# Performance work log

Measured on AMD Instinct MI355X. Metric: run time of the kernel, lower is better.

Reference implementation:

```python
import jax, jax.numpy as jnp
import numpy as np

N, E, G = 4096, 65536, 64
C_IN, PE_DIM, H, L, HEADS, C_OUT = 64, 24, 128, 2, 4, 10
HD = H // HEADS


def setup_inputs() -> dict:
    key = jax.random.key(0)
    ks = iter(jax.random.split(key, 64))

    def nrm(shape, scale=0.05):
        return jax.random.normal(next(ks), shape, jnp.float32) * scale

    inp = {}
    inp["x"] = jax.random.normal(next(ks), (N, C_IN), jnp.float32)
    inp["lap_pe"] = jax.random.normal(next(ks), (N, 8), jnp.float32)
    inp["rw_pe"] = jax.random.normal(next(ks), (N, 16), jnp.float32)
    inp["edge_index"] = jax.random.randint(next(ks), (2, E), 0, N)
    inp["batch"] = jnp.sort(jax.random.randint(next(ks), (N,), 0, G))
    inp["Wp"] = nrm((C_IN + PE_DIM, H)); inp["bp"] = jnp.zeros((H,), jnp.float32)
    inp["gin_W1"] = nrm((L, H, H)); inp["gin_b1"] = jnp.zeros((L, H), jnp.float32)
    inp["gin_W2"] = nrm((L, H, H)); inp["gin_b2"] = jnp.zeros((L, H), jnp.float32)
    inp["bn1_g"] = jnp.ones((L, H), jnp.float32); inp["bn1_b"] = jnp.zeros((L, H), jnp.float32)
    inp["bn2_g"] = jnp.ones((L, H), jnp.float32); inp["bn2_b"] = jnp.zeros((L, H), jnp.float32)
    inp["bn3_g"] = jnp.ones((L, H), jnp.float32); inp["bn3_b"] = jnp.zeros((L, H), jnp.float32)
    inp["attn_in_w"] = nrm((L, H, 3 * H)); inp["attn_in_b"] = jnp.zeros((L, 3 * H), jnp.float32)
    inp["attn_out_w"] = nrm((L, H, H)); inp["attn_out_b"] = jnp.zeros((L, H), jnp.float32)
    inp["mlp_W1"] = nrm((L, H, 2 * H)); inp["mlp_b1"] = jnp.zeros((L, 2 * H), jnp.float32)
    inp["mlp_W2"] = nrm((L, 2 * H, H)); inp["mlp_b2"] = jnp.zeros((L, H), jnp.float32)
    inp["Wr1"] = nrm((H, H)); inp["br1"] = jnp.zeros((H,), jnp.float32)
    inp["Wr2"] = nrm((H, H)); inp["br2"] = jnp.zeros((H,), jnp.float32)
    inp["Wc"] = nrm((H, C_OUT)); inp["bc"] = jnp.zeros((C_OUT,), jnp.float32)
    return inp


def _bn(x, g, b):
    # BatchNorm1d over node dim, training-mode batch statistics (biased var)
    m = jnp.mean(x, axis=0)
    v = jnp.var(x, axis=0)
    return (x - m) * jax.lax.rsqrt(v + 1e-5) * g + b


def reference(x, lap_pe, rw_pe, edge_index, batch, Wp, bp,
              gin_W1, gin_b1, gin_W2, gin_b2,
              bn1_g, bn1_b, bn2_g, bn2_b, bn3_g, bn3_b,
              attn_in_w, attn_in_b, attn_out_w, attn_out_b,
              mlp_W1, mlp_b1, mlp_W2, mlp_b2,
              Wr1, br1, Wr2, br2, Wc, bc):
    pe = jnp.concatenate([lap_pe, rw_pe], axis=-1)          # [N, 24]
    h = jnp.concatenate([x, pe], axis=-1) @ Wp + bp         # [N, H]
    src, dst = edge_index[0], edge_index[1]
    scale = 1.0 / np.sqrt(HD)
    for l in range(L):
        # --- local GINConv: (1+eps)*x_i + sum_{j->i} x_j, eps=0, then 2-layer MLP ---
        agg = jax.ops.segment_sum(h[src], dst, num_segments=N)
        g = h + agg
        g = jax.nn.relu(g @ gin_W1[l] + gin_b1[l]) @ gin_W2[l] + gin_b2[l]
        g = _bn(g + h, bn1_g[l], bn1_b[l])                  # residual + norm1
        # --- global MHA; batch is NOT forwarded to GPSConv, so all N nodes form one dense graph ---
        qkv = h @ attn_in_w[l] + attn_in_b[l]               # [N, 3H]
        q, k, v = jnp.split(qkv, 3, axis=-1)
        q = q.reshape(N, HEADS, HD).transpose(1, 0, 2)      # [Hh, N, d]
        k = k.reshape(N, HEADS, HD).transpose(1, 0, 2)
        v = v.reshape(N, HEADS, HD).transpose(1, 0, 2)
        a = jax.nn.softmax(jnp.einsum('hnd,hmd->hnm', q, k) * scale, axis=-1)
        o = jnp.einsum('hnm,hmd->hnd', a, v).transpose(1, 0, 2).reshape(N, H)
        o = o @ attn_out_w[l] + attn_out_b[l]
        o = _bn(o + h, bn2_g[l], bn2_b[l])                  # residual + norm2
        # --- combine + FFN (channels -> 2*channels -> channels) + norm3 ---
        out = g + o
        m = jax.nn.relu(out @ mlp_W1[l] + mlp_b1[l]) @ mlp_W2[l] + mlp_b2[l]
        out = _bn(out + m, bn3_g[l], bn3_b[l])
        h = jax.nn.relu(out)                                # outer F.relu in GraphGPS
    pooled = jax.ops.segment_sum(h, batch, num_segments=G)  # global_add_pool
    r = jax.nn.relu(pooled @ Wr1 + br1)
    r = jax.nn.relu(r @ Wr2 + br2)                          # dropout(0.5) disabled (eval)
    return r @ Wc + bc                                      # [G, C_OUT]
```

## Files before the change

kernel.cpp:

```cpp
#include <hip/hip_runtime.h>
#include <hip/hip_bf16.h>
#include <math.h>

#define NN 4096
#define HH 128
#define EE 65536
#define GG 64
#define KSPLIT 8
#define KLEN (NN / KSPLIT)
#define SMEM_GEMM 14336

typedef unsigned short u16;
typedef unsigned int u32;
typedef __bf16 bf16x8 __attribute__((ext_vector_type(8)));
typedef float f32x4 __attribute__((ext_vector_type(4)));

__device__ inline u16 f2b(float f) {
  u32 u = __float_as_uint(f);
  u += 0x7FFFu + ((u >> 16) & 1u);
  return (u16)(u >> 16);
}
__device__ inline u32 pkbf2(float a, float b) {
  __hip_bfloat162 h = __float22bfloat162_rn(float2{a, b});
  u32 u; __builtin_memcpy(&u, &h, 4); return u;
}

struct TDesc { const float* src; int Ks, K, M, off; };
struct TPack { TDesc d[13]; };

__global__ __launch_bounds__(256) void transcount_k(TPack P, u16* __restrict__ dst,
    const int* __restrict__ ei, int* cnt) {
  if (blockIdx.x >= 1344) {
    int e = (blockIdx.x - 1344)*256 + threadIdx.x;
    atomicAdd(&cnt[ei[EE + e]], 1);
    return;
  }
  int idx = blockIdx.x * 256 + threadIdx.x;
  for (int i = 0; i < 13; i++) {
    int sz = P.d[i].K * P.d[i].M;
    if (idx < sz) {
      int m = idx / P.d[i].K;
      int k = idx - m * P.d[i].K;
      float v = (k < P.d[i].Ks) ? P.d[i].src[(size_t)k * P.d[i].M + m] : 0.f;
      dst[P.d[i].off + idx] = f2b(v);
      return;
    }
    idx -= sz;
  }
}

__global__ __launch_bounds__(256) void scan_k(const int* __restrict__ cnt,
    int* __restrict__ rowptr, int* __restrict__ cursor) {
  __shared__ int tot[256];
  int t = threadIdx.x;
  int base = t * 16;
  int loc[16]; int s = 0;
  #pragma unroll
  for (int i = 0; i < 16; i++) { loc[i] = s; s += cnt[base + i]; }
  tot[t] = s;
  __syncthreads();
  for (int off = 1; off < 256; off <<= 1) {
    int v = (t >= off) ? tot[t - off] : 0;
    __syncthreads();
    tot[t] += v;
    __syncthreads();
  }
  int excl = (t == 0) ? 0 : tot[t - 1];
  #pragma unroll
  for (int i = 0; i < 16; i++) {
    int p = excl + loc[i];
    rowptr[base + i] = p; cursor[base + i] = p;
  }
  if (t == 255) rowptr[NN] = excl + s;
}

__global__ __launch_bounds__(256) void aggcsr_k(const int* __restrict__ rowptr,
    const int* __restrict__ elist, const float* __restrict__ h,
    float* __restrict__ agg) {
  int d = blockIdx.x*2 + (threadIdx.x >> 7);
  int c = threadIdx.x & 127;
  int beg = rowptr[d], end = rowptr[d + 1];
  float acc = 0.f;
  for (int j = beg; j < end; j++)
    acc += h[(size_t)elist[j]*HH + c];
  agg[(size_t)d*HH + c] = acc;
}

struct GArgs {
  const float *A, *A2, *A3;
  const u16* Bt;
  const float* bias;
  float* C;
  const float *res, *res2;
  float* stats;
  const float *sbase, *pg1, *pb1, *pg2, *pb2;
  const u16 *opart;
  const float *lpart;
  u16 *qb, *kb, *vt;
  int K, M;
};

template <int ASTAGE, int EPI, int RELU>
__device__ void mgemm_dev(const GArgs& a, int bx, int by, char* smem) {
  char* Ab = smem;
  char* Bb = smem + 4096;
  float* affs = (float*)(smem + 12288);
  const int tid = threadIdx.x;
  const int n0 = bx * 32, m0 = by * 64;
  const int w = tid >> 6, lane = tid & 63;
  const int g = lane >> 4, li = lane & 15;
  const int wr = w >> 1, wc = w & 1;
  const int K = a.K, M = a.M;

  if (ASTAGE == 2) {
    int plane = tid >> 7, cc = tid & 127;
    const float* st = a.sbase + plane*256;
    const float* gg = plane ? a.pg2 : a.pg1;
    const float* bb = plane ? a.pb2 : a.pb1;
    float mean = st[cc] * (1.f/NN);
    float var  = st[128+cc] * (1.f/NN) - mean*mean;
    float s = rsqrtf(var + 1e-5f) * gg[cc];
    affs[plane*256 + cc]       = s;
    affs[plane*256 + 128 + cc] = bb[cc] - mean*s;
    __syncthreads();
  }

  f32x4 acc0 = {0,0,0,0}, acc1 = {0,0,0,0};
  const int arow = tid >> 3, akseg = (tid & 7) * 8;
  const int bcol = tid >> 2, bkseg = (tid & 3) * 16;

  for (int k0 = 0; k0 < K; k0 += 64) {
    {
      float4 a0 = {0,0,0,0}, a1 = {0,0,0,0};
      if (ASTAGE == 4) {
        int n = n0 + arow;
        if (k0 == 0) {
          a0 = *(const float4*)&a.A[(size_t)n*64 + akseg];
          a1 = *(const float4*)&a.A[(size_t)n*64 + akseg + 4];
        } else {
          if (akseg == 0)       { a0 = *(const float4*)&a.A2[(size_t)n*8];
                                  a1 = *(const float4*)&a.A2[(size_t)n*8 + 4]; }
          else if (akseg == 8)  { a0 = *(const float4*)&a.A3[(size_t)n*16];
                                  a1 = *(const float4*)&a.A3[(size_t)n*16 + 4]; }
          else if (akseg == 16) { a0 = *(const float4*)&a.A3[(size_t)n*16 + 8];
                                  a1 = *(const float4*)&a.A3[(size_t)n*16 + 12]; }
        }
      } else if (ASTAGE == 3) {
        int n = n0 + arow, c = k0 + akseg;
        int head = c >> 5, d0 = c & 31;
        float4 o0 = {0,0,0,0}, o1 = {0,0,0,0}; float L = 0.f;
        #pragma unroll
        for (int s = 0; s < KSPLIT; s++) {
          const u16* ob = a.opart + ((size_t)(s*4+head)*NN + n)*32 + d0;
          uint4 xx = *(const uint4*)ob;
          o0.x += __uint_as_float(xx.x << 16);
          o0.y += __uint_as_float(xx.x & 0xffff0000u);
          o0.z += __uint_as_float(xx.y << 16);
          o0.w += __uint_as_float(xx.y & 0xffff0000u);
          o1.x += __uint_as_float(xx.z << 16);
          o1.y += __uint_as_float(xx.z & 0xffff0000u);
          o1.z += __uint_as_float(xx.w << 16);
          o1.w += __uint_as_float(xx.w & 0xffff0000u);
          L += a.lpart[(size_t)(s*4+head)*NN + n];
        }
        float inv = 1.f / L;
        a0 = make_float4(o0.x*inv, o0.y*inv, o0.z*inv, o0.w*inv);
        a1 = make_float4(o1.x*inv, o1.y*inv, o1.z*inv, o1.w*inv);
      } else {
        const float* ap = a.A + (size_t)(n0 + arow) * K + k0 + akseg;
        a0 = *(const float4*)ap; a1 = *(const float4*)(ap + 4);
        if (ASTAGE == 1) {
          const float* p2 = a.A2 + (size_t)(n0 + arow) * K + k0 + akseg;
          float4 c0 = *(const float4*)p2, c1 = *(const float4*)(p2 + 4);
          a0.x += c0.x; a0.y += c0.y; a0.z += c0.z; a0.w += c0.w;
          a1.x += c1.x; a1.y += c1.y; a1.z += c1.z; a1.w += c1.w;
        } else if (ASTAGE == 2) {
          const float* p2 = a.A2 + (size_t)(n0 + arow) * K + k0 + akseg;
          float4 c0 = *(const float4*)p2, c1 = *(const float4*)(p2 + 4);
          const float* af = affs + k0 + akseg;
          float4 s1a = *(const float4*)af,         s1b = *(const float4*)(af + 4);
          float4 t1a = *(const float4*)(af + 128), t1b = *(const float4*)(af + 132);
          float4 s2a = *(const float4*)(af + 256), s2b = *(const float4*)(af + 260);
          float4 t2a = *(const float4*)(af + 384), t2b = *(const float4*)(af + 388);
          a0.x = a0.x*s1a.x + t1a.x + c0.x*s2a.x + t2a.x;
          a0.y = a0.y*s1a.y + t1a.y + c0.y*s2a.y + t2a.y;
          a0.z = a0.z*s1a.z + t1a.z + c0.z*s2a.z + t2a.z;
          a0.w = a0.w*s1a.w + t1a.w + c0.w*s2a.w + t2a.w;
          a1.x = a1.x*s1b.x + t1b.x + c1.x*s2b.x + t2b.x;
          a1.y = a1.y*s1b.y + t1b.y + c1.y*s2b.y + t2b.y;
          a1.z = a1.z*s1b.z + t1b.z + c1.z*s2b.z + t2b.z;
          a1.w = a1.w*s1b.w + t1b.w + c1.w*s2b.w + t2b.w;
        }
      }
      u16 t8[8] = {f2b(a0.x), f2b(a0.y), f2b(a0.z), f2b(a0.w),
                   f2b(a1.x), f2b(a1.y), f2b(a1.z), f2b(a1.w)};
      *(uint4*)(Ab + ((arow*128 + akseg*2) ^ ((arow & 7) << 4))) = *(uint4*)t8;
    }
    {
      const u16* bp = a.Bt + (size_t)(m0 + bcol) * K + k0 + bkseg;
      uint4 b0 = *(const uint4*)bp;
      uint4 b1 = *(const uint4*)(bp + 8);
      int ba = bcol*128 + bkseg*2;
      int sw = (bcol & 7) << 4;
      *(uint4*)(Bb + (ba ^ sw)) = b0;
      *(uint4*)(Bb + ((ba + 16) ^ sw)) = b1;
    }
    __syncthreads();
    int row = wr*16 + li;
    int cAl = wc*32 + li, cBl = cAl + 16;
    #pragma unroll
    for (int ck = 0; ck < 2; ck++) {
      bf16x8 af = *(const bf16x8*)(Ab + ((row*128 + ck*64 + g*16) ^ ((row & 7) << 4)));
      bf16x8 bf0 = *(const bf16x8*)(Bb + ((cAl*128 + ck*64 + g*16) ^ ((cAl & 7) << 4)));
      bf16x8 bf1 = *(const bf16x8*)(Bb + ((cBl*128 + ck*64 + g*16) ^ ((cBl & 7) << 4)));
      acc0 = __builtin_amdgcn_mfma_f32_16x16x32_bf16(af, bf0, acc0, 0, 0, 0);
      acc1 = __builtin_amdgcn_mfma_f32_16x16x32_bf16(af, bf1, acc1, 0, 0, 0);
    }
    __syncthreads();
  }

  const int colA = m0 + wc*32 + li, colB = colA + 16;
  const int colAl = wc*32 + li, colBl = colAl + 16;
  const int rbase = n0 + wr*16 + 4*g;

  if (EPI == 0) {
    float b0 = a.bias[colA], b1 = a.bias[colB];
    #pragma unroll
    for (int r = 0; r < 4; r++) {
      float v0 = acc0[r] + b0, v1 = acc1[r] + b1;
      if (RELU) { v0 = fmaxf(v0, 0.f); v1 = fmaxf(v1, 0.f); }
      a.C[(size_t)(rbase + r) * M + colA] = v0;
      a.C[(size_t)(rbase + r) * M + colB] = v1;
    }
  } else if (EPI == 1 || EPI == 3) {
    float b0 = a.bias[colA], b1 = a.bias[colB];
    float sA1=0, tA1=0, sA2=0, tA2=0, sB1=0, tB1=0, sB2=0, tB2=0;
    if (EPI == 3) {
      auto mk = [&](int col, float& s1, float& t1, float& s2, float& t2) {
        float m1 = a.sbase[col]*(1.f/NN), v1 = a.sbase[128+col]*(1.f/NN) - m1*m1;
        s1 = rsqrtf(v1 + 1e-5f) * a.pg1[col]; t1 = a.pb1[col] - m1*s1;
        float m2 = a.sbase[256+col]*(1.f/NN), v2 = a.sbase[384+col]*(1.f/NN) - m2*m2;
        s2 = rsqrtf(v2 + 1e-5f) * a.pg2[col]; t2 = a.pb2[col] - m2*s2;
      };
      mk(colA, sA1, tA1, sA2, tA2);
      mk(colB, sB1, tB1, sB2, tB2);
    }
    float s0 = 0, q0 = 0, s1 = 0, q1 = 0;
    #pragma unroll
    for (int r = 0; r < 4; r++) {
      int rw2 = rbase + r;
      float v0, v1;
      if (EPI == 1) {
        v0 = acc0[r] + b0 + a.res[(size_t)rw2 * 128 + colA];
        v1 = acc1[r] + b1 + a.res[(size_t)rw2 * 128 + colB];
      } else {
        v0 = acc0[r] + b0 + a.res[(size_t)rw2*128 + colA]*sA1 + tA1
                          + a.res2[(size_t)rw2*128 + colA]*sA2 + tA2;
        v1 = acc1[r] + b1 + a.res[(size_t)rw2*128 + colB]*sB1 + tB1
                          + a.res2[(size_t)rw2*128 + colB]*sB2 + tB2;
      }
      a.C[(size_t)rw2 * M + colA] = v0;
      a.C[(size_t)rw2 * M + colB] = v1;
      s0 += v0; q0 += v0*v0; s1 += v1; q1 += v1*v1;
    }
    s0 += __shfl_xor(s0, 16); s0 += __shfl_xor(s0, 32);
    q0 += __shfl_xor(q0, 16); q0 += __shfl_xor(q0, 32);
    s1 += __shfl_xor(s1, 16); s1 += __shfl_xor(s1, 32);
    q1 += __shfl_xor(q1, 16); q1 += __shfl_xor(q1, 32);
    float* sred = (float*)smem;
    if (lane < 16) {
      sred[wr*64 + colAl] = s0;  sred[128 + wr*64 + colAl] = q0;
      sred[wr*64 + colBl] = s1;  sred[128 + wr*64 + colBl] = q1;
    }
    __syncthreads();
    if (tid < 128) {
      int c = tid & 63, isq = tid >> 6;
      float v = sred[isq*128 + c] + sred[isq*128 + 64 + c];
      atomicAdd(&a.stats[isq*128 + m0 + c], v);
    }
  } else {
    const float QS = 0.17677669529663687f * 1.4426950408889634f;
    auto doq = [&](int col, f32x4 acc, float bb) {
      if (col < 128) {
        int hd = col >> 5, d = col & 31;
        #pragma unroll
        for (int r = 0; r < 4; r++)
          a.qb[((size_t)hd*NN + rbase + r)*32 + d] = f2b((acc[r] + bb) * QS);
      } else if (col < 256) {
        int hd = (col - 128) >> 5, d = col & 31;
        #pragma unroll
        for (int r = 0; r < 4; r++)
          a.kb[((size_t)hd*NN + rbase + r)*32 + d] = f2b(acc[r] + bb);
      } else {
        #pragma unroll
        for (int r = 0; r < 4; r++)
          a.vt[(size_t)(col - 256)*NN + rbase + r] = f2b(acc[r] + bb);
      }
    };
    doq(colA, acc0, a.bias[colA]);
    doq(colB, acc1, a.bias[colB]);
  }
}

template <int AS, int EP, int RE>
__global__ __launch_bounds__(256) void k_gemm(GArgs a) {
  extern __shared__ char smem[];
  mgemm_dev<AS, EP, RE>(a, blockIdx.x, blockIdx.y, smem);
}

__global__ __launch_bounds__(256) void k_qkv_gin1(GArgs qa, GArgs ga) {
  extern __shared__ char smem[];
  int b = blockIdx.x;
  if (b < 768) mgemm_dev<0,4,0>(qa, b & 127, b >> 7, smem);
  else { b -= 768; mgemm_dev<1,0,1>(ga, b & 127, b >> 7, smem); }
}

__global__ __launch_bounds__(256) void k_gin2_ao(GArgs g2, GArgs ao) {
  extern __shared__ char smem[];
  int b = blockIdx.x;
  if (b < 256) mgemm_dev<0,1,0>(g2, b & 127, b >> 7, smem);
  else { b -= 256; mgemm_dev<3,1,0>(ao, b & 127, b >> 7, smem); }
}

__global__ __launch_bounds__(256) void k_scat_inp(const int* __restrict__ ei,
    int* cursor, int* __restrict__ elist, GArgs ia) {
  extern __shared__ char smem[];
  int b = blockIdx.x;
  if (b < 256) {
    int e = b*256 + threadIdx.x;
    int d = ei[EE + e];
    int p = atomicAdd(&cursor[d], 1);
    elist[p] = ei[e];
  } else {
    b -= 256;
    mgemm_dev<4,0,0>(ia, b & 127, b >> 7, smem);
  }
}

__global__ __launch_bounds__(256) void bn3_k(
    const float* __restrict__ out3, const float* __restrict__ stats,
    const float* __restrict__ gamma, const float* __restrict__ beta,
    float* __restrict__ h, const int* __restrict__ batch,
    float* __restrict__ pooled, int dopool) {
  int idx = blockIdx.x*256 + threadIdx.x;
  int c = idx & 127;
  float mean = stats[c] * (1.f/NN);
  float var  = stats[128+c] * (1.f/NN) - mean*mean;
  float rs = rsqrtf(var + 1e-5f);
  float r = fmaxf((out3[idx] - mean) * rs * gamma[c] + beta[c], 0.f);
  if (dopool) atomicAdd(&pooled[batch[idx >> 7]*HH + c], r);
  else        h[idx] = r;
}

__global__ __launch_bounds__(256) void mfma_attn_k(
    const u16* __restrict__ qb, const u16* __restrict__ kb,
    const u16* __restrict__ vt, u16* __restrict__ opart,
    float* __restrict__ lpart) {
  __shared__ __align__(16) u16 kbuf[2][2048];
  __shared__ __align__(16) u16 vbuf[2][2048];
  __shared__ __align__(16) u16 pbuf[4][1024];

  const int tid = threadIdx.x;
  const int w = tid >> 6, lane = tid & 63;
  const int g = lane >> 4, li = lane & 15;
  const int head = blockIdx.z;
  const int q0 = blockIdx.y * 128 + w * 16;
  const int j0 = blockIdx.x * KLEN;

  const bf16x8 qfA = *reinterpret_cast<const bf16x8*>(
      qb + ((size_t)(head*NN) + q0 + li)*32 + g*8);
  const bf16x8 qfB = *reinterpret_cast<const bf16x8*>(
      qb + ((size_t)(head*NN) + q0 + 64 + li)*32 + g*8);

  const int vd = tid >> 3;
  const int vcs = (tid & 7) ^ (vd & 7);
  const u16* kpan = kb + (size_t)head*NN*32;
  const u16* vrow_g = vt + (size_t)(head*32 + vd)*NN;

  f32x4 oA0 = {0,0,0,0}, oA1 = {0,0,0,0};
  f32x4 oB0 = {0,0,0,0}, oB1 = {0,0,0,0};
  const f32x4 zz = {0,0,0,0};
  float lsA = 0.f, lsB = 0.f;
  char* pb = (char*)&pbuf[w][0];
  const int swz = (li & 7) << 4;

  {
    uint4 kv = *(const uint4*)(kpan + (size_t)j0*32 + tid*8);
    uint4 vv = *(const uint4*)(vrow_g + j0 + vcs*8);
    *((uint4*)kbuf[0] + tid) = kv;
    *((uint4*)vbuf[0] + tid) = vv;
  }
  __syncthreads();

  const int NSTEP = KLEN / 64;
  int cur = 0;
  for (int s = 0; s < NSTEP; s++) {
    int jt = j0 + s*64;
    bool pf = (s + 1 < NSTEP);
    uint4 kv = {0,0,0,0}, vv = {0,0,0,0};
    if (pf) {
      kv = *(const uint4*)(kpan + (size_t)(jt + 64)*32 + tid*8);
      vv = *(const uint4*)(vrow_g + jt + 64 + vcs*8);
    }
    #pragma unroll
    for (int qq = 0; qq < 2; qq++) {
      const bf16x8 qf = qq ? qfB : qfA;
      f32x4 st[4];
      __builtin_amdgcn_s_setprio(1);
      #pragma unroll
      for (int t = 0; t < 4; t++) {
        bf16x8 kf = *(const bf16x8*)&kbuf[cur][(t*16 + li)*32 + g*8];
        st[t] = __builtin_amdgcn_mfma_f32_16x16x32_bf16(kf, qf, zz, 0, 0, 0);
      }
      __builtin_amdgcn_s_setprio(0);
      float lloc = 0.f;
      #pragma unroll
      for (int t = 0; t < 4; t++) {
        float p0 = exp2f(st[t][0]), p1 = exp2f(st[t][1]);
        float p2 = exp2f(st[t][2]), p3 = exp2f(st[t][3]);
        lloc += p0 + p1 + p2 + p3;
        uint2 wv2;
        wv2.x = pkbf2(p0, p1);
        wv2.y = pkbf2(p2, p3);
        *(uint2*)(pb + ((li*128 + t*32 + g*8) ^ swz)) = wv2;
      }
      if (qq) lsB += lloc; else lsA += lloc;
      __builtin_amdgcn_s_setprio(1);
      #pragma unroll
      for (int c = 0; c < 2; c++) {
        bf16x8 pa = *(const bf16x8*)(pb + ((li*128 + c*64 + g*16) ^ swz));
        int vs = ((c*4 + g) ^ (li & 7)) << 4;
        bf16x8 vb0 = *(const bf16x8*)((char*)vbuf[cur] + li*128 + vs);
        bf16x8 vb1 = *(const bf16x8*)((char*)vbuf[cur] + (16 + li)*128 + vs);
        if (qq) {
          oB0 = __builtin_amdgcn_mfma_f32_16x16x32_bf16(pa, vb0, oB0, 0, 0, 0);
          oB1 = __builtin_amdgcn_mfma_f32_16x16x32_bf16(pa, vb1, oB1, 0, 0, 0);
        } else {
          oA0 = __builtin_amdgcn_mfma_f32_16x16x32_bf16(pa, vb0, oA0, 0, 0, 0);
          oA1 = __builtin_amdgcn_mfma_f32_16x16x32_bf16(pa, vb1, oA1, 0, 0, 0);
        }
      }
      __builtin_amdgcn_s_setprio(0);
    }
    if (pf) {
      *((uint4*)kbuf[cur ^ 1] + tid) = kv;
      *((uint4*)vbuf[cur ^ 1] + tid) = vv;
    }
    __syncthreads();
    cur ^= 1;
  }
  lsA += __shfl_xor(lsA, 16);
  lsA += __shfl_xor(lsA, 32);
  lsB += __shfl_xor(lsB, 16);
  lsB += __shfl_xor(lsB, 32);

  size_t b = (size_t)(blockIdx.x*4 + head)*NN + q0;
  size_t b2 = b + 64;
  #pragma unroll
  for (int r = 0; r < 4; r++) {
    size_t ob = (b + 4*g + r)*32;
    opart[ob + li]      = f2b(oA0[r]);
    opart[ob + 16 + li] = f2b(oA1[r]);
    size_t ob2 = (b2 + 4*g + r)*32;
    opart[ob2 + li]      = f2b(oB0[r]);
    opart[ob2 + 16 + li] = f2b(oB1[r]);
  }
  if (lane < 16) {
    lpart[b + lane]  = lsA;
    lpart[b2 + lane] = lsB;
  }
}

__global__ __launch_bounds__(128) void head_k(
    const float* __restrict__ pooled,
    const float* __restrict__ Wr1, const float* __restrict__ br1,
    const float* __restrict__ Wr2, const float* __restrict__ br2,
    const float* __restrict__ Wc, const float* __restrict__ bc,
    float* __restrict__ out) {
  __shared__ float bufa[128], bufb[128];
  int g = blockIdx.x, c = threadIdx.x;
  bufa[c] = pooled[g*HH + c];
  __syncthreads();
  float acc = br1[c];
  #pragma unroll 8
  for (int k = 0; k < 128; k++) acc += bufa[k] * Wr1[k*128 + c];
  bufb[c] = fmaxf(acc, 0.f);
  __syncthreads();
  acc = br2[c];
  #pragma unroll 8
  for (int k = 0; k < 128; k++) acc += bufb[k] * Wr2[k*128 + c];
  bufa[c] = fmaxf(acc, 0.f);
  __syncthreads();
  if (c < 10) {
    acc = bc[c];
    #pragma unroll 8
    for (int k = 0; k < 128; k++) acc += bufa[k] * Wc[k*10 + c];
    out[g*10 + c] = acc;
  }
}

extern "C" void kernel_launch(void* const* d_in, const int* in_sizes, int n_in,
                              void* d_out, int out_size, void* d_ws, size_t ws_size,
                              hipStream_t stream) {
  const float* x      = (const float*)d_in[0];
  const float* lap    = (const float*)d_in[1];
  const float* rw     = (const float*)d_in[2];
  const int*   ei     = (const int*)d_in[3];
  const int*   batch  = (const int*)d_in[4];
  const float* Wp     = (const float*)d_in[5];
  const float* bp     = (const float*)d_in[6];
  const float* gin_W1 = (const float*)d_in[7];
  const float* gin_b1 = (const float*)d_in[8];
  const float* gin_W2 = (const float*)d_in[9];
  const float* gin_b2 = (const float*)d_in[10];
  const float* bn1_g  = (const float*)d_in[11];
  const float* bn1_b  = (const float*)d_in[12];
  const float* bn2_g  = (const float*)d_in[13];
  const float* bn2_b  = (const float*)d_in[14];
  const float* bn3_g  = (const float*)d_in[15];
  const float* bn3_b  = (const float*)d_in[16];
  const float* ain_w  = (const float*)d_in[17];
  const float* ain_b  = (const float*)d_in[18];
  const float* aout_w = (const float*)d_in[19];
  const float* aout_b = (const float*)d_in[20];
  const float* mlp_W1 = (const float*)d_in[21];
  const float* mlp_b1 = (const float*)d_in[22];
  const float* mlp_W2 = (const float*)d_in[23];
  const float* mlp_b2 = (const float*)d_in[24];
  const float* Wr1    = (const float*)d_in[25];
  const float* br1    = (const float*)d_in[26];
  const float* Wr2    = (const float*)d_in[27];
  const float* br2    = (const float*)d_in[28];
  const float* Wc     = (const float*)d_in[29];
  const float* bc     = (const float*)d_in[30];
  float* out = (float*)d_out;

  float* w = (float*)d_ws;
  float* h      = w + 0;
  float* agg    = w + 524288;
  float* gtmp   = w + 1048576;
  float* pre1   = w + 1572864;
  float* pre2   = w + 2097152;
  float* mlph   = w + 2621440;
  float* out3   = w + 3670016;
  u16*   opart  = (u16*)(w + 4194304);
  float* lpart  = w + 8388608;
  float* stats  = w + 8519680;
  float* pooled = w + 8521216;
  int*   cnt    = (int*)(w + 8529408);
  int*   rowptr = (int*)(w + 8533504);
  int*   cursor = (int*)(w + 8537608);
  int*   elist  = (int*)(w + 8541704);
  u16*   wts    = (u16*)(w + 8607240);
  u16*   qb     = (u16*)(w + 8779272);
  u16*   kb     = (u16*)(w + 9041416);
  u16*   vt     = (u16*)(w + 9303560);

  u16* wpt = wts;
  u16 *qkvWt[2], *g1t[2], *g2t[2], *aot[2], *m1t[2], *m2t[2];
  {
    int off = 16384;
    for (int l = 0; l < 2; l++) {
      qkvWt[l] = wts + off; off += 384*128;
      g1t[l]   = wts + off; off += 128*128;
      g2t[l]   = wts + off; off += 128*128;
      aot[l]   = wts + off; off += 128*128;
      m1t[l]   = wts + off; off += 256*128;
      m2t[l]   = wts + off; off += 128*256;
    }
  }
  TPack tp;
  {
    int ti = 0, toff = 0;
    auto addm = [&](const float* s, int Ks, int Kd, int Md) {
      tp.d[ti].src = s; tp.d[ti].Ks = Ks; tp.d[ti].K = Kd; tp.d[ti].M = Md;
      tp.d[ti].off = toff; toff += Kd * Md; ti++;
    };
    addm(Wp, 88, 128, 128);
    for (int l = 0; l < 2; l++) {
      addm(ain_w + l*HH*384, 128, 128, 384);
      addm(gin_W1 + l*HH*HH, 128, 128, 128);
      addm(gin_W2 + l*HH*HH, 128, 128, 128);
      addm(aout_w + l*HH*HH, 128, 128, 128);
      addm(mlp_W1 + l*HH*256, 128, 128, 256);
      addm(mlp_W2 + l*256*HH, 256, 256, 128);
    }
  }

  auto GA = [&](const float* A, const float* A2, const float* A3, const u16* Bt,
                const float* bias, float* C, const float* res, const float* res2,
                float* st, const float* sb, const float* g1, const float* b1,
                const float* g2, const float* b2, const u16* op, const float* lp,
                u16* q, u16* k, u16* v, int K, int M) {
    GArgs a; a.A=A; a.A2=A2; a.A3=A3; a.Bt=Bt; a.bias=bias; a.C=C; a.res=res;
    a.res2=res2; a.stats=st; a.sbase=sb; a.pg1=g1; a.pb1=b1; a.pg2=g2; a.pb2=b2;
    a.opart=op; a.lpart=lp; a.qb=q; a.kb=k; a.vt=v; a.K=K; a.M=M; return a;
  };

  hipMemsetAsync(stats, 0, 13824*sizeof(float), stream);
  transcount_k<<<1600, 256, 0, stream>>>(tp, wts, ei, cnt);
  scan_k<<<1, 256, 0, stream>>>(cnt, rowptr, cursor);
  k_scat_inp<<<512, 256, SMEM_GEMM, stream>>>(ei, cursor, elist,
      GA(x, lap, rw, wpt, bp, h, nullptr, nullptr, nullptr, nullptr,
         nullptr, nullptr, nullptr, nullptr, nullptr, nullptr,
         nullptr, nullptr, nullptr, 128, 128));

  for (int l = 0; l < 2; l++) {
    float* st1 = stats + l*768;
    float* st2 = st1 + 256;
    float* st3 = st1 + 512;

    aggcsr_k<<<NN/2, 256, 0, stream>>>(rowptr, elist, h, agg);

    k_qkv_gin1<<<1024, 256, SMEM_GEMM, stream>>>(
        GA(h, nullptr, nullptr, qkvWt[l], ain_b + l*384, nullptr, nullptr,
           nullptr, nullptr, nullptr, nullptr, nullptr, nullptr, nullptr,
           nullptr, nullptr, qb, kb, vt, 128, 384),
        GA(h, agg, nullptr, g1t[l], gin_b1 + l*HH, gtmp, nullptr, nullptr,
           nullptr, nullptr, nullptr, nullptr, nullptr, nullptr,
           nullptr, nullptr, nullptr, nullptr, nullptr, 128, 128));

    mfma_attn_k<<<dim3(KSPLIT, NN/128, 4), 256, 0, stream>>>(qb, kb, vt, opart, lpart);

    k_gin2_ao<<<512, 256, SMEM_GEMM, stream>>>(
        GA(gtmp, nullptr, nullptr, g2t[l], gin_b2 + l*HH, pre1, h, nullptr,
           st1, nullptr, nullptr, nullptr, nullptr, nullptr,
           nullptr, nullptr, nullptr, nullptr, nullptr, 128, 128),
        GA(nullptr, nullptr, nullptr, aot[l], aout_b + l*HH, pre2, h, nullptr,
           st2, nullptr, nullptr, nullptr, nullptr, nullptr,
           opart, lpart, nullptr, nullptr, nullptr, 128, 128));

    k_gemm<2,0,1><<<dim3(128,4), 256, SMEM_GEMM, stream>>>(
        GA(pre1, pre2, nullptr, m1t[l], mlp_b1 + l*256, mlph, nullptr, nullptr,
           nullptr, st1, bn1_g + l*HH, bn1_b + l*HH, bn2_g + l*HH, bn2_b + l*HH,
           nullptr, nullptr, nullptr, nullptr, nullptr, 128, 256));
    k_gemm<0,3,0><<<dim3(128,2), 256, SMEM_GEMM, stream>>>(
        GA(mlph, nullptr, nullptr, m2t[l], mlp_b2 + l*HH, out3, pre1, pre2,
           st3, st1, bn1_g + l*HH, bn1_b + l*HH, bn2_g + l*HH, bn2_b + l*HH,
           nullptr, nullptr, nullptr, nullptr, nullptr, 256, 128));
    bn3_k<<<NN*HH/256, 256, 0, stream>>>(out3, st3, bn3_g + l*HH, bn3_b + l*HH,
                                         h, batch, pooled, l == 1);
  }

  head_k<<<GG, 128, 0, stream>>>(pooled, Wr1, br1, Wr2, br2, Wc, bc, out);
}
```

Measured before the change: 187.8 us.

## Fuse post-attention GEMMs and BN3 into one cooperative kernel with grid syncs

Merges the GIN2/attention-out GEMMs, both FFN GEMMs and the BN3/ReLU/pool pass into one cooperative launch of 512 blocks, separated by grid-wide barriers. This removes three kernel launches and their inter-kernel gaps per layer. A __syncthreads is added after the stats reduction so shared memory can be reused safely across phases. The cost is grid.sync overhead, the requirement that all 512 blocks be co-resident, and idle blocks in the 256-block FFN2 phase.

New measurement: 533.0 us. 2.84x slower.

```diff
diff --git a/kernel.cpp b/kernel.cpp
--- a/kernel.cpp
+++ b/kernel.cpp
@@ -1,6 +1,9 @@
 #include <hip/hip_runtime.h>
 #include <hip/hip_bf16.h>
+#include <hip/hip_cooperative_groups.h>
 #include <math.h>
+
+namespace cg = cooperative_groups;
 
 #define NN 4096
 #define HH 128
@@ -278,6 +281,7 @@
       float v = sred[isq*128 + c] + sred[isq*128 + 64 + c];
       atomicAdd(&a.stats[isq*128 + m0 + c], v);
     }
+    __syncthreads();
   } else {
     const float QS = 0.17677669529663687f * 1.4426950408889634f;
     auto doq = [&](int col, f32x4 acc, float bb) {
@@ -302,24 +306,11 @@
   }
 }
 
-template <int AS, int EP, int RE>
-__global__ __launch_bounds__(256) void k_gemm(GArgs a) {
-  extern __shared__ char smem[];
-  mgemm_dev<AS, EP, RE>(a, blockIdx.x, blockIdx.y, smem);
-}
-
 __global__ __launch_bounds__(256) void k_qkv_gin1(GArgs qa, GArgs ga) {
   extern __shared__ char smem[];
   int b = blockIdx.x;
   if (b < 768) mgemm_dev<0,4,0>(qa, b & 127, b >> 7, smem);
   else { b -= 768; mgemm_dev<1,0,1>(ga, b & 127, b >> 7, smem); }
-}
-
-__global__ __launch_bounds__(256) void k_gin2_ao(GArgs g2, GArgs ao) {
-  extern __shared__ char smem[];
-  int b = blockIdx.x;
-  if (b < 256) mgemm_dev<0,1,0>(g2, b & 127, b >> 7, smem);
-  else { b -= 256; mgemm_dev<3,1,0>(ao, b & 127, b >> 7, smem); }
 }
 
 __global__ __launch_bounds__(256) void k_scat_inp(const int* __restrict__ ei,
@@ -337,19 +328,36 @@
   }
 }
 
-__global__ __launch_bounds__(256) void bn3_k(
-    const float* __restrict__ out3, const float* __restrict__ stats,
-    const float* __restrict__ gamma, const float* __restrict__ beta,
-    float* __restrict__ h, const int* __restrict__ batch,
-    float* __restrict__ pooled, int dopool) {
-  int idx = blockIdx.x*256 + threadIdx.x;
-  int c = idx & 127;
-  float mean = stats[c] * (1.f/NN);
-  float var  = stats[128+c] * (1.f/NN) - mean*mean;
-  float rs = rsqrtf(var + 1e-5f);
-  float r = fmaxf((out3[idx] - mean) * rs * gamma[c] + beta[c], 0.f);
-  if (dopool) atomicAdd(&pooled[batch[idx >> 7]*HH + c], r);
-  else        h[idx] = r;
+struct BackArgs {
+  GArgs g2, ao, f1, f2;
+  const float* bn3g; const float* bn3b;
+  float* h; const int* batch; float* pooled;
+  const float* st3; const float* out3;
+  int dopool;
+};
+
+__global__ __launch_bounds__(256) void layer_back_k(BackArgs ba) {
+  extern __shared__ char smem[];
+  cg::grid_group grid = cg::this_grid();
+  int b = blockIdx.x;
+  if (b < 256) mgemm_dev<0,1,0>(ba.g2, b & 127, b >> 7, smem);
+  else { int bb = b - 256; mgemm_dev<3,1,0>(ba.ao, bb & 127, bb >> 7, smem); }
+  grid.sync();
+  mgemm_dev<2,0,1>(ba.f1, b & 127, b >> 7, smem);
+  grid.sync();
+  if (b < 256) mgemm_dev<0,3,0>(ba.f2, b & 127, b >> 7, smem);
+  grid.sync();
+  #pragma unroll
+  for (int i = 0; i < 4; i++) {
+    int idx = (i*512 + b)*256 + threadIdx.x;
+    int c = idx & 127;
+    float mean = ba.st3[c] * (1.f/NN);
+    float var  = ba.st3[128+c] * (1.f/NN) - mean*mean;
+    float rs = rsqrtf(var + 1e-5f);
+    float r = fmaxf((ba.out3[idx] - mean) * rs * ba.bn3g[c] + ba.bn3b[c], 0.f);
+    if (ba.dopool) atomicAdd(&ba.pooled[ba.batch[idx >> 7]*HH + c], r);
+    else           ba.h[idx] = r;
+  }
 }
 
 __global__ __launch_bounds__(256) void mfma_attn_k(
@@ -622,24 +630,26 @@
 
     mfma_attn_k<<<dim3(KSPLIT, NN/128, 4), 256, 0, stream>>>(qb, kb, vt, opart, lpart);
 
-    k_gin2_ao<<<512, 256, SMEM_GEMM, stream>>>(
-        GA(gtmp, nullptr, nullptr, g2t[l], gin_b2 + l*HH, pre1, h, nullptr,
-           st1, nullptr, nullptr, nullptr, nullptr, nullptr,
-           nullptr, nullptr, nullptr, nullptr, nullptr, 128, 128),
-        GA(nullptr, nullptr, nullptr, aot[l], aout_b + l*HH, pre2, h, nullptr,
-           st2, nullptr, nullptr, nullptr, nullptr, nullptr,
-           opart, lpart, nullptr, nullptr, nullptr, 128, 128));
-
-    k_gemm<2,0,1><<<dim3(128,4), 256, SMEM_GEMM, stream>>>(
-        GA(pre1, pre2, nullptr, m1t[l], mlp_b1 + l*256, mlph, nullptr, nullptr,
-           nullptr, st1, bn1_g + l*HH, bn1_b + l*HH, bn2_g + l*HH, bn2_b + l*HH,
-           nullptr, nullptr, nullptr, nullptr, nullptr, 128, 256));
-    k_gemm<0,3,0><<<dim3(128,2), 256, SMEM_GEMM, stream>>>(
-        GA(mlph, nullptr, nullptr, m2t[l], mlp_b2 + l*HH, out3, pre1, pre2,
-           st3, st1, bn1_g + l*HH, bn1_b + l*HH, bn2_g + l*HH, bn2_b + l*HH,
-           nullptr, nullptr, nullptr, nullptr, nullptr, 256, 128));
-    bn3_k<<<NN*HH/256, 256, 0, stream>>>(out3, st3, bn3_g + l*HH, bn3_b + l*HH,
-                                         h, batch, pooled, l == 1);
+    BackArgs ba;
+    ba.g2 = GA(gtmp, nullptr, nullptr, g2t[l], gin_b2 + l*HH, pre1, h, nullptr,
+               st1, nullptr, nullptr, nullptr, nullptr, nullptr,
+               nullptr, nullptr, nullptr, nullptr, nullptr, 128, 128);
+    ba.ao = GA(nullptr, nullptr, nullptr, aot[l], aout_b + l*HH, pre2, h, nullptr,
+               st2, nullptr, nullptr, nullptr, nullptr, nullptr,
+               opart, lpart, nullptr, nullptr, nullptr, 128, 128);
+    ba.f1 = GA(pre1, pre2, nullptr, m1t[l], mlp_b1 + l*256, mlph, nullptr, nullptr,
+               nullptr, st1, bn1_g + l*HH, bn1_b + l*HH, bn2_g + l*HH, bn2_b + l*HH,
+               nullptr, nullptr, nullptr, nullptr, nullptr, 128, 256);
+    ba.f2 = GA(mlph, nullptr, nullptr, m2t[l], mlp_b2 + l*HH, out3, pre1, pre2,
+               st3, st1, bn1_g + l*HH, bn1_b + l*HH, bn2_g + l*HH, bn2_b + l*HH,
+               nullptr, nullptr, nullptr, nullptr, nullptr, 256, 128);
+    ba.bn3g = bn3_g + l*HH; ba.bn3b = bn3_b + l*HH;
+    ba.h = h; ba.batch = batch; ba.pooled = pooled;
+    ba.st3 = st3; ba.out3 = out3;
+    ba.dopool = (l == 1);
+    void* kargs[] = { &ba };
+    hipLaunchCooperativeKernel((void*)layer_back_k, dim3(512), dim3(256),
+                               kargs, SMEM_GEMM, stream);
   }
 
   head_k<<<GG, 128, 0, stream>>>(pooled, Wr1, br1, Wr2, br2, Wc, bc, out);
```

## Apply GIN first linear before neighbor aggregation to drop the aggregation kernel

Applied to the files above, without the earlier changes.

Uses linearity: (h + sum of neighbors) @ W1 equals h@W1 plus the sum of neighbor rows of h@W1. The first GIN GEMM now runs on h alone with a zero bias, and the second GIN GEMM's A-load gathers and sums the transformed rows over the CSR edge list, then adds the bias and applies ReLU before converting to bf16. This removes the separate aggregation launch and the agg buffer round-trip. In exchange the gather moves into the GEMM A-staging loop, where its irregular edge loop may stall the tile load, and the neighbor sums are taken after the bf16 GEMM rather than before it, which changes rounding.

After: 199.5 us. +6.3%, slower.

```diff
diff --git a/kernel.cpp b/kernel.cpp
--- a/kernel.cpp
+++ b/kernel.cpp
@@ -74,18 +74,6 @@
   if (t == 255) rowptr[NN] = excl + s;
 }
 
-__global__ __launch_bounds__(256) void aggcsr_k(const int* __restrict__ rowptr,
-    const int* __restrict__ elist, const float* __restrict__ h,
-    float* __restrict__ agg) {
-  int d = blockIdx.x*2 + (threadIdx.x >> 7);
-  int c = threadIdx.x & 127;
-  int beg = rowptr[d], end = rowptr[d + 1];
-  float acc = 0.f;
-  for (int j = beg; j < end; j++)
-    acc += h[(size_t)elist[j]*HH + c];
-  agg[(size_t)d*HH + c] = acc;
-}
-
 struct GArgs {
   const float *A, *A2, *A3;
   const u16* Bt;
@@ -97,6 +85,8 @@
   const u16 *opart;
   const float *lpart;
   u16 *qb, *kb, *vt;
+  const int *rowptr, *elist;
+  const float* abias;
   int K, M;
 };
 
@@ -166,15 +156,27 @@
         float inv = 1.f / L;
         a0 = make_float4(o0.x*inv, o0.y*inv, o0.z*inv, o0.w*inv);
         a1 = make_float4(o1.x*inv, o1.y*inv, o1.z*inv, o1.w*inv);
+      } else if (ASTAGE == 5) {
+        int n = n0 + arow;
+        const float* tp = a.A + (size_t)n*128 + k0 + akseg;
+        a0 = *(const float4*)tp; a1 = *(const float4*)(tp + 4);
+        int beg = a.rowptr[n], end = a.rowptr[n + 1];
+        for (int j = beg; j < end; j++) {
+          const float* sp = a.A + (size_t)a.elist[j]*128 + k0 + akseg;
+          float4 s0 = *(const float4*)sp, s1 = *(const float4*)(sp + 4);
+          a0.x += s0.x; a0.y += s0.y; a0.z += s0.z; a0.w += s0.w;
+          a1.x += s1.x; a1.y += s1.y; a1.z += s1.z; a1.w += s1.w;
+        }
+        float4 bb0 = *(const float4*)&a.abias[k0 + akseg];
+        float4 bb1 = *(const float4*)&a.abias[k0 + akseg + 4];
+        a0.x = fmaxf(a0.x + bb0.x, 0.f); a0.y = fmaxf(a0.y + bb0.y, 0.f);
+        a0.z = fmaxf(a0.z + bb0.z, 0.f); a0.w = fmaxf(a0.w + bb0.w, 0.f);
+        a1.x = fmaxf(a1.x + bb1.x, 0.f); a1.y = fmaxf(a1.y + bb1.y, 0.f);
+        a1.z = fmaxf(a1.z + bb1.z, 0.f); a1.w = fmaxf(a1.w + bb1.w, 0.f);
       } else {
         const float* ap = a.A + (size_t)(n0 + arow) * K + k0 + akseg;
         a0 = *(const float4*)ap; a1 = *(const float4*)(ap + 4);
-        if (ASTAGE == 1) {
-          const float* p2 = a.A2 + (size_t)(n0 + arow) * K + k0 + akseg;
-          float4 c0 = *(const float4*)p2, c1 = *(const float4*)(p2 + 4);
-          a0.x += c0.x; a0.y += c0.y; a0.z += c0.z; a0.w += c0.w;
-          a1.x += c1.x; a1.y += c1.y; a1.z += c1.z; a1.w += c1.w;
-        } else if (ASTAGE == 2) {
+        if (ASTAGE == 2) {
           const float* p2 = a.A2 + (size_t)(n0 + arow) * K + k0 + akseg;
           float4 c0 = *(const float4*)p2, c1 = *(const float4*)(p2 + 4);
           const float* af = affs + k0 + akseg;
@@ -312,13 +314,13 @@
   extern __shared__ char smem[];
   int b = blockIdx.x;
   if (b < 768) mgemm_dev<0,4,0>(qa, b & 127, b >> 7, smem);
-  else { b -= 768; mgemm_dev<1,0,1>(ga, b & 127, b >> 7, smem); }
+  else { b -= 768; mgemm_dev<0,0,0>(ga, b & 127, b >> 7, smem); }
 }
 
 __global__ __launch_bounds__(256) void k_gin2_ao(GArgs g2, GArgs ao) {
   extern __shared__ char smem[];
   int b = blockIdx.x;
-  if (b < 256) mgemm_dev<0,1,0>(g2, b & 127, b >> 7, smem);
+  if (b < 256) mgemm_dev<5,1,0>(g2, b & 127, b >> 7, smem);
   else { b -= 256; mgemm_dev<3,1,0>(ao, b & 127, b >> 7, smem); }
 }
 
@@ -537,7 +539,6 @@
 
   float* w = (float*)d_ws;
   float* h      = w + 0;
-  float* agg    = w + 524288;
   float* gtmp   = w + 1048576;
   float* pre1   = w + 1572864;
   float* pre2   = w + 2097152;
@@ -548,13 +549,14 @@
   float* stats  = w + 8519680;
   float* pooled = w + 8521216;
   int*   cnt    = (int*)(w + 8529408);
-  int*   rowptr = (int*)(w + 8533504);
-  int*   cursor = (int*)(w + 8537608);
-  int*   elist  = (int*)(w + 8541704);
-  u16*   wts    = (u16*)(w + 8607240);
-  u16*   qb     = (u16*)(w + 8779272);
-  u16*   kb     = (u16*)(w + 9041416);
-  u16*   vt     = (u16*)(w + 9303560);
+  float* zbias  = w + 8533504;
+  int*   rowptr = (int*)(w + 8533632);
+  int*   cursor = (int*)(w + 8537736);
+  int*   elist  = (int*)(w + 8541832);
+  u16*   wts    = (u16*)(w + 8607368);
+  u16*   qb     = (u16*)(w + 8779400);
+  u16*   kb     = (u16*)(w + 9041544);
+  u16*   vt     = (u16*)(w + 9303688);
 
   u16* wpt = wts;
   u16 *qkvWt[2], *g1t[2], *g2t[2], *aot[2], *m1t[2], *m2t[2];
@@ -594,10 +596,11 @@
                 u16* q, u16* k, u16* v, int K, int M) {
     GArgs a; a.A=A; a.A2=A2; a.A3=A3; a.Bt=Bt; a.bias=bias; a.C=C; a.res=res;
     a.res2=res2; a.stats=st; a.sbase=sb; a.pg1=g1; a.pb1=b1; a.pg2=g2; a.pb2=b2;
-    a.opart=op; a.lpart=lp; a.qb=q; a.kb=k; a.vt=v; a.K=K; a.M=M; return a;
+    a.opart=op; a.lpart=lp; a.qb=q; a.kb=k; a.vt=v;
+    a.rowptr=nullptr; a.elist=nullptr; a.abias=nullptr; a.K=K; a.M=M; return a;
   };
 
-  hipMemsetAsync(stats, 0, 13824*sizeof(float), stream);
+  hipMemsetAsync(stats, 0, 13952*sizeof(float), stream);
   transcount_k<<<1600, 256, 0, stream>>>(tp, wts, ei, cnt);
   scan_k<<<1, 256, 0, stream>>>(cnt, rowptr, cursor);
   k_scat_inp<<<512, 256, SMEM_GEMM, stream>>>(ei, cursor, elist,
@@ -610,22 +613,22 @@
     float* st2 = st1 + 256;
     float* st3 = st1 + 512;
 
-    aggcsr_k<<<NN/2, 256, 0, stream>>>(rowptr, elist, h, agg);
-
     k_qkv_gin1<<<1024, 256, SMEM_GEMM, stream>>>(
         GA(h, nullptr, nullptr, qkvWt[l], ain_b + l*384, nullptr, nullptr,
            nullptr, nullptr, nullptr, nullptr, nullptr, nullptr, nullptr,
            nullptr, nullptr, qb, kb, vt, 128, 384),
-        GA(h, agg, nullptr, g1t[l], gin_b1 + l*HH, gtmp, nullptr, nullptr,
+        GA(h, nullptr, nullptr, g1t[l], zbias, gtmp, nullptr, nullptr,
            nullptr, nullptr, nullptr, nullptr, nullptr, nullptr,
            nullptr, nullptr, nullptr, nullptr, nullptr, 128, 128));
 
     mfma_attn_k<<<dim3(KSPLIT, NN/128, 4), 256, 0, stream>>>(qb, kb, vt, opart, lpart);
 
+    GArgs g2a = GA(gtmp, nullptr, nullptr, g2t[l], gin_b2 + l*HH, pre1, h, nullptr,
+                   st1, nullptr, nullptr, nullptr, nullptr, nullptr,
+                   nullptr, nullptr, nullptr, nullptr, nullptr, 128, 128);
+    g2a.rowptr = rowptr; g2a.elist = elist; g2a.abias = gin_b1 + l*HH;
     k_gin2_ao<<<512, 256, SMEM_GEMM, stream>>>(
-        GA(gtmp, nullptr, nullptr, g2t[l], gin_b2 + l*HH, pre1, h, nullptr,
-           st1, nullptr, nullptr, nullptr, nullptr, nullptr,
-           nullptr, nullptr, nullptr, nullptr, nullptr, 128, 128),
+        g2a,
         GA(nullptr, nullptr, nullptr, aot[l], aout_b + l*HH, pre2, h, nullptr,
            st2, nullptr, nullptr, nullptr, nullptr, nullptr,
            opart, lpart, nullptr, nullptr, nullptr, 128, 128));
```
